# Performance work log

Measured on AMD Instinct MI355X. Metric: run time of the kernel, lower is better.

## Reference

```python
import jax, jax.numpy as jnp
import numpy as np

N, E, D_IN, D_OUT = 50000, 1600000, 256, 256


def setup_inputs() -> dict:
    key = jax.random.key(0)
    k1, k2, k3, k4, k5, k6 = jax.random.split(key, 6)
    x = jax.random.normal(k1, (N, D_IN), dtype=jnp.float32)
    edge_index = jax.random.randint(k2, (2, E), 0, N, dtype=jnp.int64)
    s = 1.0 / np.sqrt(D_IN)
    W1 = jax.random.uniform(k3, (D_OUT, D_IN), minval=-s, maxval=s, dtype=jnp.float32)
    b1 = jax.random.uniform(k4, (D_OUT,), minval=-s, maxval=s, dtype=jnp.float32)
    W2 = jax.random.uniform(k5, (D_OUT, D_IN), minval=-s, maxval=s, dtype=jnp.float32)
    b2 = jax.random.uniform(k6, (D_OUT,), minval=-s, maxval=s, dtype=jnp.float32)
    return {"x": x, "W1": W1, "b1": b1, "W2": W2, "b2": b2, "edge_index": edge_index}


def reference(x, W1, b1, W2, b2, edge_index):
    # edge_index[0] = destination node, edge_index[1] = neighbor (as in the torch loop)
    dst = edge_index[0]
    nbr = edge_index[1]
    n = x.shape[0]
    # segment mean of neighbor features per destination node
    agg = jax.ops.segment_sum(x[nbr], dst, num_segments=n)  # [N, D_IN]
    cnt = jax.ops.segment_sum(jnp.ones((nbr.shape[0],), x.dtype), dst, num_segments=n)
    mean = agg / jnp.maximum(cnt, 1.0)[:, None]  # isolated nodes -> 0 (torch gives NaN)
    return x @ W1.T + b1 + mean @ W2.T + b2
```

## Files before the change

kernel.cpp:

```cpp
#include <hip/hip_runtime.h>
#include <hip/hip_bf16.h>
#include <hip/hip_fp8.h>

typedef __bf16 bf16x4 __attribute__((ext_vector_type(4)));
typedef __bf16 bf16x8 __attribute__((ext_vector_type(8)));
typedef float f32x4 __attribute__((ext_vector_type(4)));
typedef float f32x2 __attribute__((ext_vector_type(2)));

#define D_IN 256
#define D_OUT 256
#define K_DIM 512
#define PAD 96
#define NBIN 640
#define NPS 79
#define ROUND1 3072
#define CAP3 12
#define CVT_BLK 1024
#define CONVW_BLK 512


__device__ __forceinline__ unsigned int pack4_fp8(float a, float b, float c, float d) {
#if __has_builtin(__builtin_amdgcn_cvt_pk_fp8_f32)
    int r = 0;
    r = __builtin_amdgcn_cvt_pk_fp8_f32(a, b, r, false);
    r = __builtin_amdgcn_cvt_pk_fp8_f32(c, d, r, true);
    return (unsigned int)r;
#else
    union { unsigned int u; unsigned char by[4]; } v;
    v.by[0] = __hip_fp8_e4m3(a).__x;
    v.by[1] = __hip_fp8_e4m3(b).__x;
    v.by[2] = __hip_fp8_e4m3(c).__x;
    v.by[3] = __hip_fp8_e4m3(d).__x;
    return v.u;
#endif
}

__device__ __forceinline__ void unpack4_fp8(unsigned int u, f32x2& lo, f32x2& hi) {
#if __has_builtin(__builtin_amdgcn_cvt_pk_f32_fp8)
    lo = __builtin_amdgcn_cvt_pk_f32_fp8(u, false);
    hi = __builtin_amdgcn_cvt_pk_f32_fp8(u, true);
#else
    union { unsigned int uu; unsigned char by[4]; } v; v.uu = u;
    __hip_fp8_e4m3 q0, q1, q2, q3;
    q0.__x = v.by[0]; q1.__x = v.by[1]; q2.__x = v.by[2]; q3.__x = v.by[3];
    lo[0] = (float)q0; lo[1] = (float)q1; hi[0] = (float)q2; hi[1] = (float)q3;
#endif
}


__global__ __launch_bounds__(256) void prep_kernel(const int* __restrict__ dst,
                                                   unsigned int* __restrict__ hist,
                                                   const float* __restrict__ x,
                                                   unsigned int* __restrict__ x8,
                                                   __bf16* __restrict__ xb,
                                                   const float* __restrict__ W1,
                                                   const float* __restrict__ W2,
                                                   const float* __restrict__ b1,
                                                   const float* __restrict__ b2,
                                                   __bf16* __restrict__ Wbuf,
                                                   float* __restrict__ bias,
                                                   int E, int n8, int nSub) {
    __shared__ int bcnt[NBIN];
    const int tid = threadIdx.x;
    const int bid = blockIdx.x;

    if (bid < nSub) {
        for (int s = tid; s < NBIN; s += 256) bcnt[s] = 0;
        __syncthreads();
        const int base = bid * ROUND1;
        const int hi = min(E, base + ROUND1);
        for (int e = base + tid; e < hi; e += 256) {
            int d = __builtin_nontemporal_load(dst + e);
            atomicAdd(&bcnt[d / NPS], 1);
        }
        __syncthreads();
        for (int s = tid; s < NBIN; s += 256)
            hist[(size_t)bid * NBIN + s] = (unsigned int)bcnt[s];
    } else if (bid < nSub + CVT_BLK) {
        int i = (bid - nSub) * 256 + tid;
        for (; i < n8; i += CVT_BLK * 256) {
            const float4* p = (const float4*)(x + (size_t)i * 8);
            float4 a = p[0], b = p[1];
            uint2 o;
            o.x = pack4_fp8(a.x, a.y, a.z, a.w);
            o.y = pack4_fp8(b.x, b.y, b.z, b.w);
            *(uint2*)(x8 + (size_t)i * 2) = o;
            bf16x8 hb = { (__bf16)a.x, (__bf16)a.y, (__bf16)a.z, (__bf16)a.w,
                          (__bf16)b.x, (__bf16)b.y, (__bf16)b.z, (__bf16)b.w };
            *(bf16x8*)(xb + (size_t)i * 8) = hb;
        }
    } else {
        int i = (bid - nSub - CVT_BLK) * 256 + tid;
        int o = i >> 9;
        int k = i & 511;
        float v = (k < D_IN) ? W1[o * D_IN + k] : W2[o * D_IN + (k - D_IN)];
        Wbuf[i] = (__bf16)v;
        if (i < D_OUT) bias[i] = b1[i] + b2[i];
    }
}


__global__ __launch_bounds__(64) void scan_kernel(const unsigned int* __restrict__ hist,
                                                  unsigned int* __restrict__ sbase,
                                                  int* __restrict__ bin_cnt, int nSub) {
    const int s = blockIdx.x;
    const int lane = threadIdx.x;
    unsigned int carry = 0;
    for (int b0 = 0; b0 < nSub; b0 += 64) {
        int b = b0 + lane;
        unsigned int v = (b < nSub) ? hist[(size_t)b * NBIN + s] : 0u;
        unsigned int sc = v;
        #pragma unroll
        for (int d = 1; d < 64; d <<= 1) {
            unsigned int t = __shfl_up(sc, d, 64);
            if (lane >= d) sc += t;
        }
        if (b < nSub) sbase[(size_t)b * NBIN + s] = carry + sc - v;
        carry += __shfl(sc, 63, 64);
    }
    if (lane == 0) bin_cnt[s] = (int)carry;
}


__global__ __launch_bounds__(512) void place_kernel(const int* __restrict__ dst,
                                                    const int* __restrict__ nbr,
                                                    const unsigned int* __restrict__ sbase,
                                                    unsigned int* __restrict__ bins,
                                                    int E, int segCap, int nSub) {
    __shared__ unsigned int buf[NBIN][CAP3];
    __shared__ int bcnt[NBIN];
    __shared__ unsigned int gbase[NBIN];
    const int tid = threadIdx.x;
    const int bid = blockIdx.x;

    for (int s = tid; s < NBIN; s += 512) {
        bcnt[s] = 0;
        gbase[s] = sbase[(size_t)bid * NBIN + s];
    }
    __syncthreads();

    const int base = bid * ROUND1;
    const int hi = min(E, base + ROUND1);
    for (int e = base + tid; e < hi; e += 512) {
        int d  = __builtin_nontemporal_load(dst + e);
        int nb = __builtin_nontemporal_load(nbr + e);
        int s = d / NPS;
        unsigned int packed = ((unsigned int)d << 16) | (unsigned int)nb;
        int pos = atomicAdd(&bcnt[s], 1);
        if (pos < CAP3) buf[s][pos] = packed;
        else bins[(size_t)s * segCap + gbase[s] + pos] = packed;
    }
    __syncthreads();

    const int wave = tid >> 6, lane = tid & 63;
    for (int s = wave; s < NBIN; s += 8) {
        int c = min(bcnt[s], CAP3);
        if (lane < c) bins[(size_t)s * segCap + gbase[s] + lane] = buf[s][lane];
    }
}


__global__ __launch_bounds__(512) void fillgather_kernel(const unsigned int* __restrict__ x8,
                                                         const unsigned int* __restrict__ bins,
                                                         const int* __restrict__ bin_cnt,
                                                         __bf16* __restrict__ Mbuf,
                                                         int segCap, int N) {
    __shared__ unsigned short lbuck[NPS][PAD];
    __shared__ int lcnt[NPS];
    const int s = blockIdx.x;
    const int node0 = s * NPS;
    const int tid = threadIdx.x;

    for (int i = tid; i < NPS; i += 512) lcnt[i] = 0;
    __syncthreads();

    const int cnt = min(bin_cnt[s], segCap);
    const size_t sbase_ = (size_t)s * segCap;
    for (int i = tid; i < cnt; i += 512) {
        unsigned int p = bins[sbase_ + i];
        int nl = (int)(p >> 16) - node0;
        int pos = atomicAdd(&lcnt[nl], 1);
        if (pos < PAD) lbuck[nl][pos] = (unsigned short)(p & 0xffffu);
    }
    __syncthreads();

    const int wave = tid >> 6, lane = tid & 63;
    for (int nl = wave; nl < NPS; nl += 8) {
        int node = node0 + nl;
        if (node >= N) continue;
        int c = min(lcnt[nl], PAD);
        const unsigned int* bw = (const unsigned int*)(&lbuck[nl][0]);

        f32x2 a0lo = {0.f,0.f}, a0hi = {0.f,0.f};
        f32x2 a1lo = {0.f,0.f}, a1hi = {0.f,0.f};
        f32x2 a2lo = {0.f,0.f}, a2hi = {0.f,0.f};
        f32x2 a3lo = {0.f,0.f}, a3hi = {0.f,0.f};

        int i = 0;
        for (; i + 16 <= c; i += 16) {
            int ib = i >> 1;
            unsigned int w0 = bw[ib+0], w1 = bw[ib+1], w2 = bw[ib+2], w3 = bw[ib+3];
            unsigned int w4 = bw[ib+4], w5 = bw[ib+5], w6 = bw[ib+6], w7 = bw[ib+7];
            unsigned int u0  = x8[(size_t)(w0 & 0xffffu) * 64 + lane];
            unsigned int u1  = x8[(size_t)(w0 >> 16)     * 64 + lane];
            unsigned int u2  = x8[(size_t)(w1 & 0xffffu) * 64 + lane];
            unsigned int u3  = x8[(size_t)(w1 >> 16)     * 64 + lane];
            unsigned int u4  = x8[(size_t)(w2 & 0xffffu) * 64 + lane];
            unsigned int u5  = x8[(size_t)(w2 >> 16)     * 64 + lane];
            unsigned int u6  = x8[(size_t)(w3 & 0xffffu) * 64 + lane];
            unsigned int u7  = x8[(size_t)(w3 >> 16)     * 64 + lane];
            unsigned int u8  = x8[(size_t)(w4 & 0xffffu) * 64 + lane];
            unsigned int u9  = x8[(size_t)(w4 >> 16)     * 64 + lane];
            unsigned int u10 = x8[(size_t)(w5 & 0xffffu) * 64 + lane];
            unsigned int u11 = x8[(size_t)(w5 >> 16)     * 64 + lane];
            unsigned int u12 = x8[(size_t)(w6 & 0xffffu) * 64 + lane];
            unsigned int u13 = x8[(size_t)(w6 >> 16)     * 64 + lane];
            unsigned int u14 = x8[(size_t)(w7 & 0xffffu) * 64 + lane];
            unsigned int u15 = x8[(size_t)(w7 >> 16)     * 64 + lane];
            f32x2 lo, hi;
            unpack4_fp8(u0,  lo, hi); a0lo += lo; a0hi += hi;
            unpack4_fp8(u1,  lo, hi); a1lo += lo; a1hi += hi;
            unpack4_fp8(u2,  lo, hi); a2lo += lo; a2hi += hi;
            unpack4_fp8(u3,  lo, hi); a3lo += lo; a3hi += hi;
            unpack4_fp8(u4,  lo, hi); a0lo += lo; a0hi += hi;
            unpack4_fp8(u5,  lo, hi); a1lo += lo; a1hi += hi;
            unpack4_fp8(u6,  lo, hi); a2lo += lo; a2hi += hi;
            unpack4_fp8(u7,  lo, hi); a3lo += lo; a3hi += hi;
            unpack4_fp8(u8,  lo, hi); a0lo += lo; a0hi += hi;
            unpack4_fp8(u9,  lo, hi); a1lo += lo; a1hi += hi;
            unpack4_fp8(u10, lo, hi); a2lo += lo; a2hi += hi;
            unpack4_fp8(u11, lo, hi); a3lo += lo; a3hi += hi;
            unpack4_fp8(u12, lo, hi); a0lo += lo; a0hi += hi;
            unpack4_fp8(u13, lo, hi); a1lo += lo; a1hi += hi;
            unpack4_fp8(u14, lo, hi); a2lo += lo; a2hi += hi;
            unpack4_fp8(u15, lo, hi); a3lo += lo; a3hi += hi;
        }
        for (; i + 4 <= c; i += 4) {
            int ib = i >> 1;
            unsigned int w0 = bw[ib+0], w1 = bw[ib+1];
            unsigned int u0 = x8[(size_t)(w0 & 0xffffu) * 64 + lane];
            unsigned int u1 = x8[(size_t)(w0 >> 16)     * 64 + lane];
            unsigned int u2 = x8[(size_t)(w1 & 0xffffu) * 64 + lane];
            unsigned int u3 = x8[(size_t)(w1 >> 16)     * 64 + lane];
            f32x2 lo, hi;
            unpack4_fp8(u0, lo, hi); a0lo += lo; a0hi += hi;
            unpack4_fp8(u1, lo, hi); a1lo += lo; a1hi += hi;
            unpack4_fp8(u2, lo, hi); a2lo += lo; a2hi += hi;
            unpack4_fp8(u3, lo, hi); a3lo += lo; a3hi += hi;
        }
        for (; i < c; i++) {
            unsigned int u0 = x8[(size_t)lbuck[nl][i] * 64 + lane];
            f32x2 lo, hi;
            unpack4_fp8(u0, lo, hi); a0lo += lo; a0hi += hi;
        }
        a0lo += a1lo + a2lo + a3lo;
        a0hi += a1hi + a2hi + a3hi;
        float inv = (c > 0) ? 1.0f / (float)c : 0.0f;
        bf16x4 hm = { (__bf16)(a0lo[0] * inv), (__bf16)(a0lo[1] * inv),
                      (__bf16)(a0hi[0] * inv), (__bf16)(a0hi[1] * inv) };
        *(bf16x4*)(Mbuf + (size_t)node * D_IN + lane * 4) = hm;
    }
}


__global__ __launch_bounds__(512) void gemm_kernel(const __bf16* __restrict__ xb,
                                                   const __bf16* __restrict__ Mb,
                                                   const __bf16* __restrict__ W,
                                                   const float* __restrict__ bias,
                                                   float* __restrict__ out, int M) {
    __shared__ __bf16 As[64][72];
    __shared__ __bf16 Ws[256][72];

    const int tid = threadIdx.x;
    const int lane = tid & 63;
    const int wave = tid >> 6;
    const int wr = wave >> 2;
    const int wc = wave & 3;
    const int brow = blockIdx.x * 64;

    f32x4 acc[2][4];
    #pragma unroll
    for (int m = 0; m < 2; m++)
        #pragma unroll
        for (int n = 0; n < 4; n++)
            acc[m][n] = (f32x4){0.f, 0.f, 0.f, 0.f};

    const int lr = lane & 15;
    const int lg8 = (lane >> 4) * 8;

    const int rowA = tid >> 3;
    const int chA  = (tid & 7) * 8;
    const int growA = brow + rowA;
    const bool aOK = (growA < M);
    const int chW = (tid & 7) * 8;

    bf16x8 rA = {};
    bf16x8 rW[4];

    if (aOK) rA = *(const bf16x8*)(xb + (size_t)growA * D_IN + chA);
    #pragma unroll
    for (int r = 0; r < 4; r++) {
        int rowW = (r * 512 + tid) >> 3;
        rW[r] = *(const bf16x8*)(W + (size_t)rowW * K_DIM + chW);
    }

    for (int kk = 0; kk < 8; kk++) {
        *(bf16x8*)(&As[rowA][chA]) = rA;
        #pragma unroll
        for (int r = 0; r < 4; r++) {
            int rowW = (r * 512 + tid) >> 3;
            *(bf16x8*)(&Ws[rowW][chW]) = rW[r];
        }
        __syncthreads();

        if (kk < 7) {
            const int kn = (kk + 1) * 64;
            const __bf16* srcA = (kn < D_IN) ? xb : Mb;
            if (aOK) rA = *(const bf16x8*)(srcA + (size_t)growA * D_IN + (kn & (D_IN - 1)) + chA);
            #pragma unroll
            for (int r = 0; r < 4; r++) {
                int rowW = (r * 512 + tid) >> 3;
                rW[r] = *(const bf16x8*)(W + (size_t)rowW * K_DIM + kn + chW);
            }
        }

        #pragma unroll
        for (int kq = 0; kq < 2; kq++) {
            const int co = kq * 32 + lg8;
            bf16x8 af[2], wf[4];
            #pragma unroll
            for (int m = 0; m < 2; m++) af[m] = *(const bf16x8*)(&As[wr * 32 + m * 16 + lr][co]);
            #pragma unroll
            for (int n = 0; n < 4; n++) wf[n] = *(const bf16x8*)(&Ws[wc * 64 + n * 16 + lr][co]);
            #pragma unroll
            for (int m = 0; m < 2; m++)
                #pragma unroll
                for (int n = 0; n < 4; n++)
                    acc[m][n] = __builtin_amdgcn_mfma_f32_16x16x32_bf16(af[m], wf[n], acc[m][n], 0, 0, 0);
        }
        __syncthreads();
    }

    const int lg = lane >> 4;
    #pragma unroll
    for (int nf = 0; nf < 4; nf++) {
        int col = wc * 64 + nf * 16 + lr;
        float bv = bias[col];
        #pragma unroll
        for (int mf = 0; mf < 2; mf++) {
            int row0 = brow + wr * 32 + mf * 16 + lg * 4;
            #pragma unroll
            for (int j = 0; j < 4; j++) {
                int row = row0 + j;
                if (row < M) out[(size_t)row * D_OUT + col] = acc[mf][nf][j] + bv;
            }
        }
    }
}


extern "C" void kernel_launch(void* const* d_in, const int* in_sizes, int n_in,
                              void* d_out, int out_size, void* d_ws, size_t ws_size,
                              hipStream_t stream) {
    const float* x  = (const float*)d_in[0];
    const float* W1 = (const float*)d_in[1];
    const float* b1 = (const float*)d_in[2];
    const float* W2 = (const float*)d_in[3];
    const float* b2 = (const float*)d_in[4];
    const int* edges = (const int*)d_in[5];

    const int N = in_sizes[0] / D_IN;
    const int E = in_sizes[5] / 2;
    const int* dst = edges;
    const int* nbr = edges + E;
    const int segCap = (E / NBIN) * 3 / 2 + 64;
    const int nSub = (E + ROUND1 - 1) / ROUND1;
    const int n8 = N * D_IN / 8;

    char* ws = (char*)d_ws;
    size_t woff = 0;
    auto alloc = [&](size_t bytes) -> void* {
        void* p = ws + woff;
        woff = (woff + bytes + 255) & ~(size_t)255;
        return p;
    };
    unsigned int* x8 = (unsigned int*)alloc((size_t)N * D_IN);
    __bf16* xb   = (__bf16*)alloc((size_t)N * D_IN * 2);
    __bf16* Mbuf = (__bf16*)alloc((size_t)N * D_IN * 2);
    __bf16* Wbuf = (__bf16*)alloc((size_t)D_OUT * K_DIM * 2);
    float*  bias = (float*)alloc(D_OUT * 4);
    int* bin_cnt = (int*)alloc(NBIN * 4);
    unsigned int* hist  = (unsigned int*)alloc((size_t)nSub * NBIN * 4);
    unsigned int* sbase = (unsigned int*)alloc((size_t)nSub * NBIN * 4);
    unsigned int* bins  = (unsigned int*)alloc((size_t)NBIN * segCap * 4);

    prep_kernel<<<nSub + CVT_BLK + CONVW_BLK, 256, 0, stream>>>(
        dst, hist, x, x8, xb, W1, W2, b1, b2, Wbuf, bias, E, n8, nSub);
    scan_kernel<<<NBIN, 64, 0, stream>>>(hist, sbase, bin_cnt, nSub);
    place_kernel<<<nSub, 512, 0, stream>>>(dst, nbr, sbase, bins, E, segCap, nSub);

    int fgBlocks = (N + NPS - 1) / NPS;
    fillgather_kernel<<<fgBlocks, 512, 0, stream>>>(x8, bins, bin_cnt, Mbuf, segCap, N);

    int nblk = (N + 63) / 64;
    gemm_kernel<<<nblk, 512, 0, stream>>>(xb, Mbuf, Wbuf, bias, (float*)d_out, N);
}
```

Before: 136.9 us.

## Double GEMM row tile to 128 and retune binning granularity

The GEMM block now covers 128 rows instead of 64, with each wave computing a 64x64 tile. The weight tile is now shared by twice as many rows, which halves the weight traffic per output row. The weight register prefetch is dropped and W is loaded straight into LDS each k-step, and launch bounds request 4 blocks per SM. Separately, the bin count goes up and nodes-per-block goes down for the binning and gather kernels (NBIN 1250, NPS 40, CAP3 8), which changes load balance in the aggregation phase. The risks are more register pressure from 64 accumulators and exposed W load latency.

```diff
diff --git a/kernel.cpp b/kernel.cpp
--- a/kernel.cpp
+++ b/kernel.cpp
@@ -11,10 +11,10 @@
 #define D_OUT 256
 #define K_DIM 512
 #define PAD 96
-#define NBIN 640
-#define NPS 79
+#define NBIN 1250
+#define NPS 40
 #define ROUND1 3072
-#define CAP3 12
+#define CAP3 8
 #define CVT_BLK 1024
 #define CONVW_BLK 512
 
@@ -263,12 +263,12 @@
 }
 
 
-__global__ __launch_bounds__(512) void gemm_kernel(const __bf16* __restrict__ xb,
-                                                   const __bf16* __restrict__ Mb,
-                                                   const __bf16* __restrict__ W,
-                                                   const float* __restrict__ bias,
-                                                   float* __restrict__ out, int M) {
-    __shared__ __bf16 As[64][72];
+__global__ __launch_bounds__(512, 4) void gemm_kernel(const __bf16* __restrict__ xb,
+                                                      const __bf16* __restrict__ Mb,
+                                                      const __bf16* __restrict__ W,
+                                                      const float* __restrict__ bias,
+                                                      float* __restrict__ out, int M) {
+    __shared__ __bf16 As[128][72];
     __shared__ __bf16 Ws[256][72];
 
     const int tid = threadIdx.x;
@@ -276,11 +276,11 @@
     const int wave = tid >> 6;
     const int wr = wave >> 2;
     const int wc = wave & 3;
-    const int brow = blockIdx.x * 64;
-
-    f32x4 acc[2][4];
+    const int brow = blockIdx.x * 128;
+
+    f32x4 acc[4][4];
     #pragma unroll
-    for (int m = 0; m < 2; m++)
+    for (int m = 0; m < 4; m++)
         #pragma unroll
         for (int n = 0; n < 4; n++)
             acc[m][n] = (f32x4){0.f, 0.f, 0.f, 0.f};
@@ -288,52 +288,48 @@
     const int lr = lane & 15;
     const int lg8 = (lane >> 4) * 8;
 
-    const int rowA = tid >> 3;
+    const int rowA0 = tid >> 3;
+    const int rowA1 = 64 + (tid >> 3);
     const int chA  = (tid & 7) * 8;
-    const int growA = brow + rowA;
-    const bool aOK = (growA < M);
+    const int growA0 = brow + rowA0;
+    const int growA1 = brow + rowA1;
+    const bool aOK0 = (growA0 < M);
+    const bool aOK1 = (growA1 < M);
     const int chW = (tid & 7) * 8;
 
-    bf16x8 rA = {};
-    bf16x8 rW[4];
-
-    if (aOK) rA = *(const bf16x8*)(xb + (size_t)growA * D_IN + chA);
-    #pragma unroll
-    for (int r = 0; r < 4; r++) {
-        int rowW = (r * 512 + tid) >> 3;
-        rW[r] = *(const bf16x8*)(W + (size_t)rowW * K_DIM + chW);
-    }
+    bf16x8 rA0 = {}, rA1 = {};
+    if (aOK0) rA0 = *(const bf16x8*)(xb + (size_t)growA0 * D_IN + chA);
+    if (aOK1) rA1 = *(const bf16x8*)(xb + (size_t)growA1 * D_IN + chA);
 
     for (int kk = 0; kk < 8; kk++) {
-        *(bf16x8*)(&As[rowA][chA]) = rA;
+        const int k0 = kk * 64;
         #pragma unroll
         for (int r = 0; r < 4; r++) {
             int rowW = (r * 512 + tid) >> 3;
-            *(bf16x8*)(&Ws[rowW][chW]) = rW[r];
-        }
+            *(bf16x8*)(&Ws[rowW][chW]) = *(const bf16x8*)(W + (size_t)rowW * K_DIM + k0 + chW);
+        }
+        *(bf16x8*)(&As[rowA0][chA]) = rA0;
+        *(bf16x8*)(&As[rowA1][chA]) = rA1;
         __syncthreads();
 
         if (kk < 7) {
-            const int kn = (kk + 1) * 64;
+            const int kn = k0 + 64;
             const __bf16* srcA = (kn < D_IN) ? xb : Mb;
-            if (aOK) rA = *(const bf16x8*)(srcA + (size_t)growA * D_IN + (kn & (D_IN - 1)) + chA);
-            #pragma unroll
-            for (int r = 0; r < 4; r++) {
-                int rowW = (r * 512 + tid) >> 3;
-                rW[r] = *(const bf16x8*)(W + (size_t)rowW * K_DIM + kn + chW);
-            }
+            const int knm = kn & (D_IN - 1);
+            if (aOK0) rA0 = *(const bf16x8*)(srcA + (size_t)growA0 * D_IN + knm + chA);
+            if (aOK1) rA1 = *(const bf16x8*)(srcA + (size_t)growA1 * D_IN + knm + chA);
         }
 
         #pragma unroll
         for (int kq = 0; kq < 2; kq++) {
             const int co = kq * 32 + lg8;
-            bf16x8 af[2], wf[4];
+            bf16x8 af[4], wf[4];
             #pragma unroll
-            for (int m = 0; m < 2; m++) af[m] = *(const bf16x8*)(&As[wr * 32 + m * 16 + lr][co]);
+            for (int m = 0; m < 4; m++) af[m] = *(const bf16x8*)(&As[wr * 64 + m * 16 + lr][co]);
             #pragma unroll
             for (int n = 0; n < 4; n++) wf[n] = *(const bf16x8*)(&Ws[wc * 64 + n * 16 + lr][co]);
             #pragma unroll
-            for (int m = 0; m < 2; m++)
+            for (int m = 0; m < 4; m++)
                 #pragma unroll
                 for (int n = 0; n < 4; n++)
                     acc[m][n] = __builtin_amdgcn_mfma_f32_16x16x32_bf16(af[m], wf[n], acc[m][n], 0, 0, 0);
@@ -347,8 +343,8 @@
         int col = wc * 64 + nf * 16 + lr;
         float bv = bias[col];
         #pragma unroll
-        for (int mf = 0; mf < 2; mf++) {
-            int row0 = brow + wr * 32 + mf * 16 + lg * 4;
+        for (int mf = 0; mf < 4; mf++) {
+            int row0 = brow + wr * 64 + mf * 16 + lg * 4;
             #pragma unroll
             for (int j = 0; j < 4; j++) {
                 int row = row0 + j;
@@ -402,6 +398,6 @@
     int fgBlocks = (N + NPS - 1) / NPS;
     fillgather_kernel<<<fgBlocks, 512, 0, stream>>>(x8, bins, bin_cnt, Mbuf, segCap, N);
 
-    int nblk = (N + 63) / 64;
+    int nblk = (N + 127) / 128;
     gemm_kernel<<<nblk, 512, 0, stream>>>(xb, Mbuf, Wbuf, bias, (float*)d_out, N);
 }
```

Result: slower. 141.1 us (+3.1%).
